# Performance work log

Measured on AMD Instinct MI355X. Metric: run time of the kernel, lower is better.

The kernel has to match this reference:

```python
import jax, jax.numpy as jnp
import numpy as np

N_NODES = 50000
N_EDGES = 800000
H = 128
LN_EPS = 1e-5


def setup_inputs() -> dict:
    key = jax.random.key(0)
    ks = jax.random.split(key, 8)
    x = jax.random.normal(ks[0], (N_NODES, H), dtype=jnp.float32)
    edge_index = jax.random.randint(ks[1], (2, N_EDGES), 0, N_NODES, dtype=jnp.int64)
    # edge_attention MLP params: Linear(2H -> H), ReLU, Linear(H -> 1), Sigmoid
    W1 = jax.random.normal(ks[2], (2 * H, H), dtype=jnp.float32) * 0.02
    b1 = jnp.zeros((H,), dtype=jnp.float32)
    W2 = jax.random.normal(ks[3], (H, 1), dtype=jnp.float32) * 0.02
    b2 = jnp.zeros((1,), dtype=jnp.float32)
    # LayerNorm affine params
    gamma = jnp.ones((H,), dtype=jnp.float32)
    beta = jnp.zeros((H,), dtype=jnp.float32)
    return {"x": x, "edge_index": edge_index, "W1": W1, "b1": b1,
            "W2": W2, "b2": b2, "gamma": gamma, "beta": beta}


def reference(x, edge_index, W1, b1, W2, b2, gamma, beta):
    src = edge_index[0]
    tgt = edge_index[1]
    # per-edge gated weight: sigmoid(MLP([x_src, x_tgt]))  -> [E]
    edge_feat = jnp.concatenate([x[src], x[tgt]], axis=1)        # [E, 2H]
    h = jax.nn.relu(edge_feat @ W1 + b1)                          # [E, H]
    w = jax.nn.sigmoid(h @ W2 + b2)[:, 0]                         # [E]
    # scatter-add weighted source features into targets (fused replacement
    # for the per-node Python loop in the original)
    agg = jax.ops.segment_sum(w[:, None] * x[src], tgt,
                              num_segments=x.shape[0])            # [N, H]
    attended = x + agg
    # LayerNorm over last dim
    mu = jnp.mean(attended, axis=-1, keepdims=True)
    var = jnp.mean(jnp.square(attended - mu), axis=-1, keepdims=True)
    out = (attended - mu) * jax.lax.rsqrt(var + LN_EPS) * gamma + beta
    return out
```

## Files before the change

### kernel.cpp

```cpp
#include <hip/hip_runtime.h>

static __device__ __forceinline__ unsigned short f2bf(float f) {
    union { float f; unsigned int u; } c; c.f = f;
    unsigned int u = c.u;
    return (unsigned short)((u + 0x7FFFu + ((u >> 16) & 1u)) >> 16);
}
static __device__ __forceinline__ float bflo(unsigned int uu) {
    union { unsigned int u; float f; } c; c.u = uu << 16; return c.f;
}
static __device__ __forceinline__ float bfhi(unsigned int uu) {
    union { unsigned int u; float f; } c; c.u = uu & 0xffff0000u; return c.f;
}
static __device__ __forceinline__ unsigned char f2fp8(float f) {
    int enc = __builtin_amdgcn_cvt_pk_fp8_f32(f, f, 0, false);
    return (unsigned char)(enc & 0xff);
}

typedef __bf16 bf16x8 __attribute__((ext_vector_type(8)));
typedef float  f32x4  __attribute__((ext_vector_type(4)));
typedef float  f32x2  __attribute__((ext_vector_type(2)));

#define SLOT      64
#define SPILLCAP  8192

static __device__ __forceinline__ float mlp16(uint4 ua, const float* __restrict__ vf,
                                              const float* __restrict__ w2r) {
    f32x2 d0 = __builtin_amdgcn_cvt_pk_f32_fp8(ua.x, false);
    f32x2 d1 = __builtin_amdgcn_cvt_pk_f32_fp8(ua.x, true);
    f32x2 d2 = __builtin_amdgcn_cvt_pk_f32_fp8(ua.y, false);
    f32x2 d3 = __builtin_amdgcn_cvt_pk_f32_fp8(ua.y, true);
    f32x2 d4 = __builtin_amdgcn_cvt_pk_f32_fp8(ua.z, false);
    f32x2 d5 = __builtin_amdgcn_cvt_pk_f32_fp8(ua.z, true);
    f32x2 d6 = __builtin_amdgcn_cvt_pk_f32_fp8(ua.w, false);
    f32x2 d7 = __builtin_amdgcn_cvt_pk_f32_fp8(ua.w, true);
    float p = 0.0f;
    p = fmaf(fmaxf(d0.x + vf[0],  0.f), w2r[0],  p);
    p = fmaf(fmaxf(d0.y + vf[1],  0.f), w2r[1],  p);
    p = fmaf(fmaxf(d1.x + vf[2],  0.f), w2r[2],  p);
    p = fmaf(fmaxf(d1.y + vf[3],  0.f), w2r[3],  p);
    p = fmaf(fmaxf(d2.x + vf[4],  0.f), w2r[4],  p);
    p = fmaf(fmaxf(d2.y + vf[5],  0.f), w2r[5],  p);
    p = fmaf(fmaxf(d3.x + vf[6],  0.f), w2r[6],  p);
    p = fmaf(fmaxf(d3.y + vf[7],  0.f), w2r[7],  p);
    p = fmaf(fmaxf(d4.x + vf[8],  0.f), w2r[8],  p);
    p = fmaf(fmaxf(d4.y + vf[9],  0.f), w2r[9],  p);
    p = fmaf(fmaxf(d5.x + vf[10], 0.f), w2r[10], p);
    p = fmaf(fmaxf(d5.y + vf[11], 0.f), w2r[11], p);
    p = fmaf(fmaxf(d6.x + vf[12], 0.f), w2r[12], p);
    p = fmaf(fmaxf(d6.y + vf[13], 0.f), w2r[13], p);
    p = fmaf(fmaxf(d7.x + vf[14], 0.f), w2r[14], p);
    p = fmaf(fmaxf(d7.y + vf[15], 0.f), w2r[15], p);
    return p;
}

__global__ void k_prep3(const float* __restrict__ W1, unsigned short* __restrict__ Bt,
                        const float* __restrict__ x, unsigned short* __restrict__ XB,
                        int* __restrict__ degnsp, int NH4, int N) {
    int idx = blockIdx.x * blockDim.x + threadIdx.x;
    int T = gridDim.x * blockDim.x;

    if (idx < 256 * 128) {
        int j = idx >> 7, k = idx & 127;
        int r = (j < 128) ? k : (128 + k);
        Bt[idx] = f2bf(W1[r * 128 + (j & 127)]);
    }

    for (int i = idx; i < NH4; i += T) {
        float4 f = ((const float4*)x)[i];
        ushort4 o;
        o.x = f2bf(f.x); o.y = f2bf(f.y); o.z = f2bf(f.z); o.w = f2bf(f.w);
        ((ushort4*)XB)[i] = o;
    }

    for (int i = idx; i <= N; i += T) degnsp[i] = 0;
}

template <typename IT>
__global__ __launch_bounds__(256) void k_gemmsc(const unsigned short* __restrict__ XB,
                                                const unsigned short* __restrict__ Bt,
                                                const float* __restrict__ b1,
                                                unsigned char* __restrict__ U,
                                                unsigned short* __restrict__ V,
                                                const int* __restrict__ ei,
                                                int* __restrict__ degnsp,
                                                IT* __restrict__ esrc2,
                                                int* __restrict__ spt,
                                                int* __restrict__ sps,
                                                int M, int E) {
    int wave = threadIdx.x >> 6, lane = threadIdx.x & 63;
    int row0 = blockIdx.x * 64 + wave * 16;
    int col0 = blockIdx.y * 64;
    int lr = lane & 15;
    int lk = (lane >> 4) << 3;

    f32x4 acc[4] = {};
    int arow = row0 + lr;
    bool in = (arow < M);
    const unsigned short* xr = XB + (size_t)arow * 128;

#pragma unroll
    for (int kk = 0; kk < 4; ++kk) {
        int k = kk * 32 + lk;
        bf16x8 a = {};
        if (in) a = *(const bf16x8*)(xr + k);
#pragma unroll
        for (int nf = 0; nf < 4; ++nf) {
            int col = col0 + nf * 16 + lr;
            bf16x8 b = *(const bf16x8*)(Bt + col * 128 + k);
            acc[nf] = __builtin_amdgcn_mfma_f32_16x16x32_bf16(a, b, acc[nf], 0, 0, 0);
        }
    }
    int rb = row0 + ((lane >> 4) << 2);
    if (col0 < 128) {
#pragma unroll
        for (int nf = 0; nf < 4; ++nf) {
            int feat = col0 + nf * 16 + lr;
#pragma unroll
            for (int r = 0; r < 4; ++r) {
                int node = rb + r;
                if (node < M) U[(size_t)node * 128 + feat] = f2fp8(acc[nf][r]);
            }
        }
    } else {
#pragma unroll
        for (int nf = 0; nf < 4; ++nf) {
            int feat = col0 + nf * 16 + lr - 128;
            float bias = b1[feat];
#pragma unroll
            for (int r = 0; r < 4; ++r) {
                int node = rb + r;
                if (node < M) V[(size_t)node * 128 + feat] = f2bf(acc[nf][r] + bias);
            }
        }
    }

    int gtid = ((blockIdx.y * gridDim.x + blockIdx.x) * blockDim.x) + threadIdx.x;
    int T = gridDim.x * gridDim.y * blockDim.x;
    int N = M;
    for (int e = gtid; e < E; e += T) {
        int s = ei[e];
        int t = ei[E + e];
        int r = atomicAdd(degnsp + t, 1);
        if (r < SLOT) {
            esrc2[((size_t)t << 6) + r] = (IT)s;
        } else {
            int sp = atomicAdd(degnsp + N, 1);
            if (sp < SPILLCAP) { spt[sp] = t; sps[sp] = s; }
        }
    }
}

template <typename IT>
__global__ __launch_bounds__(256) void k_fused_slot(const unsigned char* __restrict__ U,
                                                    const unsigned short* __restrict__ V,
                                                    const unsigned short* __restrict__ XB,
                                                    const int* __restrict__ degnsp,
                                                    const IT* __restrict__ esrc2,
                                                    const int* __restrict__ spt,
                                                    const int* __restrict__ sps,
                                                    const float* __restrict__ W2,
                                                    const float* __restrict__ b2,
                                                    const float* __restrict__ gamma,
                                                    const float* __restrict__ beta,
                                                    float* __restrict__ out, int N) {
    int row = blockIdx.x * 4 + (threadIdx.x >> 6);
    if (row >= N) return;
    int lane = threadIdx.x & 63;
    int el = lane & 7;
    int q  = lane >> 3;

    float w2r[16];
#pragma unroll
    for (int i = 0; i < 16; ++i) w2r[i] = W2[16 * q + i];
    float b2s = b2[0];

    const unsigned short* vp = V + (size_t)row * 128 + 16 * q;
    uint4 va = *(const uint4*)vp;
    uint4 vb = *(const uint4*)(vp + 8);
    float vf[16];
    vf[0]  = bflo(va.x); vf[1]  = bfhi(va.x);
    vf[2]  = bflo(va.y); vf[3]  = bfhi(va.y);
    vf[4]  = bflo(va.z); vf[5]  = bfhi(va.z);
    vf[6]  = bflo(va.w); vf[7]  = bfhi(va.w);
    vf[8]  = bflo(vb.x); vf[9]  = bfhi(vb.x);
    vf[10] = bflo(vb.y); vf[11] = bfhi(vb.y);
    vf[12] = bflo(vb.z); vf[13] = bfhi(vb.z);
    vf[14] = bflo(vb.w); vf[15] = bfhi(vb.w);

    int dg = degnsp[row];
    int st = row << 6;
    int en = st + (dg < SLOT ? dg : SLOT);

    unsigned int xvr = *(const unsigned int*)(XB + (size_t)row * 128 + 2 * lane);
    float a0 = bflo(xvr), a1 = bfhi(xvr);

    for (int g = st; g < en; g += 8) {
        int e = g + el;
        bool val = (e < en);
        int s = val ? (int)esrc2[e] : 0;

        uint4 ua = *(const uint4*)(U + (size_t)s * 128 + 16 * q);
        float p = mlp16(ua, vf, w2r);
        p += __shfl_xor(p, 8);
        p += __shfl_xor(p, 16);
        p += __shfl_xor(p, 32);
        float w = val ? 1.0f / (1.0f + __expf(-(p + b2s))) : 0.0f;

#pragma unroll
        for (int j = 0; j < 8; ++j) {
            float wj = __shfl(w, j);
            int   sj = __shfl(s, j);
            unsigned int xv = *(const unsigned int*)(XB + (size_t)sj * 128 + 2 * lane);
            a0 = fmaf(wj, bflo(xv), a0);
            a1 = fmaf(wj, bfhi(xv), a1);
        }
    }

    int ns = degnsp[N];
    if (ns > 0) {
        if (ns > SPILLCAP) ns = SPILLCAP;
        for (int i = 0; i < ns; ++i) {
            if (spt[i] == row) {
                int s = sps[i];
                uint4 ua = *(const uint4*)(U + (size_t)s * 128 + 16 * q);
                float p = mlp16(ua, vf, w2r);
                p += __shfl_xor(p, 8);
                p += __shfl_xor(p, 16);
                p += __shfl_xor(p, 32);
                float w = 1.0f / (1.0f + __expf(-(p + b2s)));
                unsigned int xv = *(const unsigned int*)(XB + (size_t)s * 128 + 2 * lane);
                a0 = fmaf(w, bflo(xv), a0);
                a1 = fmaf(w, bfhi(xv), a1);
            }
        }
    }

    float sm = a0 + a1;
#pragma unroll
    for (int off = 32; off; off >>= 1) sm += __shfl_xor(sm, off);
    float mu = sm * (1.0f / 128.0f);
    float d0v = a0 - mu, d1v = a1 - mu;
    float qq = d0v * d0v + d1v * d1v;
#pragma unroll
    for (int off = 32; off; off >>= 1) qq += __shfl_xor(qq, off);
    float rstd = rsqrtf(qq * (1.0f / 128.0f) + 1e-5f);
    float2 gg = *(const float2*)(gamma + 2 * lane);
    float2 bb = *(const float2*)(beta + 2 * lane);
    float2 o;
    o.x = d0v * rstd * gg.x + bb.x;
    o.y = d1v * rstd * gg.y + bb.y;
    *(float2*)(out + (size_t)row * 128 + 2 * lane) = o;
}

extern "C" void kernel_launch(void* const* d_in, const int* in_sizes, int n_in,
                              void* d_out, int out_size, void* d_ws, size_t ws_size,
                              hipStream_t stream) {
    const float* x     = (const float*)d_in[0];
    const int*   ei    = (const int*)d_in[1];
    const float* W1    = (const float*)d_in[2];
    const float* b1    = (const float*)d_in[3];
    const float* W2    = (const float*)d_in[4];
    const float* b2    = (const float*)d_in[5];
    const float* gamma = (const float*)d_in[6];
    const float* beta  = (const float*)d_in[7];
    float* out = (float*)d_out;

    const int N = in_sizes[0] / 128;
    const int E = in_sizes[1] / 2;

    char* w = (char*)d_ws;
    size_t off = 0;
    auto alloc = [&](size_t bytes) {
        char* p = w + off;
        off = (off + bytes + 255) & ~(size_t)255;
        return p;
    };
    unsigned short* Bt = (unsigned short*)alloc(256 * 128 * 2);
    unsigned char*  U  = (unsigned char*)alloc((size_t)N * 128);
    unsigned short* V  = (unsigned short*)alloc((size_t)N * 128 * 2);
    unsigned short* XB = (unsigned short*)alloc((size_t)N * 128 * 2);
    int* degnsp = (int*)alloc((size_t)(N + 1) * 4);
    int* spt    = (int*)alloc((size_t)SPILLCAP * 4);
    int* sps    = (int*)alloc((size_t)SPILLCAP * 4);

    bool small_idx = (N <= 65535);
    void* esrc2v;
    if (small_idx) esrc2v = alloc((size_t)N * SLOT * 2);
    else           esrc2v = alloc((size_t)N * SLOT * 4);

    k_prep3<<<2048, 256, 0, stream>>>(W1, Bt, x, XB, degnsp, N * 128 / 4, N);

    dim3 ggrid((N + 63) / 64, 4);
    if (small_idx) {
        unsigned short* esrc2 = (unsigned short*)esrc2v;
        k_gemmsc<unsigned short><<<ggrid, 256, 0, stream>>>(XB, Bt, b1, U, V, ei,
                                                            degnsp, esrc2, spt, sps,
                                                            N, E);
        k_fused_slot<unsigned short><<<(N + 3) / 4, 256, 0, stream>>>(
            U, V, XB, degnsp, esrc2, spt, sps, W2, b2, gamma, beta, out, N);
    } else {
        int* esrc2 = (int*)esrc2v;
        k_gemmsc<int><<<ggrid, 256, 0, stream>>>(XB, Bt, b1, U, V, ei,
                                                 degnsp, esrc2, spt, sps, N, E);
        k_fused_slot<int><<<(N + 3) / 4, 256, 0, stream>>>(
            U, V, XB, degnsp, esrc2, spt, sps, W2, b2, gamma, beta, out, N);
    }
}
```

Measured before the change: 152.4 us.

## Partition edge bucketing by target range per XCD with chunked work queues

The edge-to-slot scatter inside the GEMM kernel now reads the hardware XCC id. Each XCD owns one eighth of the target-node range and pulls 1024-edge chunks from its own atomic cursor, so the degree atomics and slot writes for a given node stay within one XCD's L2. The per-node counter atomics are relaxed to workgroup scope. In exchange every XCD scans the full target index array, and correctness now depends on the XCC id being in 0..7 and on these narrower-scope atomics being coherent across workgroups.

```diff
diff --git a/kernel.cpp b/kernel.cpp
--- a/kernel.cpp
+++ b/kernel.cpp
@@ -15,6 +15,11 @@
     int enc = __builtin_amdgcn_cvt_pk_fp8_f32(f, f, 0, false);
     return (unsigned char)(enc & 0xff);
 }
+static __device__ __forceinline__ int xcc_id() {
+    unsigned v;
+    asm volatile("s_getreg_b32 %0, hwreg(HW_REG_XCC_ID, 0, 32)" : "=s"(v));
+    return (int)(v & 7u);
+}
 
 typedef __bf16 bf16x8 __attribute__((ext_vector_type(8)));
 typedef float  f32x4  __attribute__((ext_vector_type(4)));
@@ -22,6 +27,8 @@
 
 #define SLOT      64
 #define SPILLCAP  8192
+#define NXCD      8
+#define CHUNK     1024
 
 static __device__ __forceinline__ float mlp16(uint4 ua, const float* __restrict__ vf,
                                               const float* __restrict__ w2r) {
@@ -55,7 +62,8 @@
 
 __global__ void k_prep3(const float* __restrict__ W1, unsigned short* __restrict__ Bt,
                         const float* __restrict__ x, unsigned short* __restrict__ XB,
-                        int* __restrict__ degnsp, int NH4, int N) {
+                        int* __restrict__ degnsp, int* __restrict__ cursor,
+                        int NH4, int N) {
     int idx = blockIdx.x * blockDim.x + threadIdx.x;
     int T = gridDim.x * blockDim.x;
 
@@ -64,6 +72,7 @@
         int r = (j < 128) ? k : (128 + k);
         Bt[idx] = f2bf(W1[r * 128 + (j & 127)]);
     }
+    if (idx < NXCD) cursor[idx] = 0;
 
     for (int i = idx; i < NH4; i += T) {
         float4 f = ((const float4*)x)[i];
@@ -83,6 +92,7 @@
                                                 unsigned short* __restrict__ V,
                                                 const int* __restrict__ ei,
                                                 int* __restrict__ degnsp,
+                                                int* __restrict__ cursor,
                                                 IT* __restrict__ esrc2,
                                                 int* __restrict__ spt,
                                                 int* __restrict__ sps,
@@ -134,18 +144,31 @@
         }
     }
 
-    int gtid = ((blockIdx.y * gridDim.x + blockIdx.x) * blockDim.x) + threadIdx.x;
-    int T = gridDim.x * gridDim.y * blockDim.x;
     int N = M;
-    for (int e = gtid; e < E; e += T) {
-        int s = ei[e];
-        int t = ei[E + e];
-        int r = atomicAdd(degnsp + t, 1);
-        if (r < SLOT) {
-            esrc2[((size_t)t << 6) + r] = (IT)s;
-        } else {
-            int sp = atomicAdd(degnsp + N, 1);
-            if (sp < SPILLCAP) { spt[sp] = t; sps[sp] = s; }
+    int cls = xcc_id();
+    int t0 = (int)(((long long)N * cls) >> 3);
+    int t1 = (int)(((long long)N * (cls + 1)) >> 3);
+    int nchunk = (E + CHUNK - 1) / CHUNK;
+
+    for (;;) {
+        int c;
+        if (lane == 0) c = atomicAdd(cursor + cls, 1);
+        c = __shfl(c, 0);
+        if (c >= nchunk) break;
+        int e0 = c * CHUNK;
+        int e1 = e0 + CHUNK; if (e1 > E) e1 = E;
+        for (int e = e0 + lane; e < e1; e += 64) {
+            int t = ei[E + e];
+            if (t < t0 || t >= t1) continue;
+            int s = ei[e];
+            int r = __hip_atomic_fetch_add(degnsp + t, 1, __ATOMIC_RELAXED,
+                                           __HIP_MEMORY_SCOPE_WORKGROUP);
+            if (r < SLOT) {
+                esrc2[((size_t)t << 6) + r] = (IT)s;
+            } else {
+                int sp = atomicAdd(degnsp + N, 1);
+                if (sp < SPILLCAP) { spt[sp] = t; sps[sp] = s; }
+            }
         }
     }
 }
@@ -280,6 +303,7 @@
     unsigned short* V  = (unsigned short*)alloc((size_t)N * 128 * 2);
     unsigned short* XB = (unsigned short*)alloc((size_t)N * 128 * 2);
     int* degnsp = (int*)alloc((size_t)(N + 1) * 4);
+    int* cursor = (int*)alloc(NXCD * 4);
     int* spt    = (int*)alloc((size_t)SPILLCAP * 4);
     int* sps    = (int*)alloc((size_t)SPILLCAP * 4);
 
@@ -288,20 +312,22 @@
     if (small_idx) esrc2v = alloc((size_t)N * SLOT * 2);
     else           esrc2v = alloc((size_t)N * SLOT * 4);
 
-    k_prep3<<<2048, 256, 0, stream>>>(W1, Bt, x, XB, degnsp, N * 128 / 4, N);
+    k_prep3<<<2048, 256, 0, stream>>>(W1, Bt, x, XB, degnsp, cursor,
+                                      N * 128 / 4, N);
 
     dim3 ggrid((N + 63) / 64, 4);
     if (small_idx) {
         unsigned short* esrc2 = (unsigned short*)esrc2v;
         k_gemmsc<unsigned short><<<ggrid, 256, 0, stream>>>(XB, Bt, b1, U, V, ei,
-                                                            degnsp, esrc2, spt, sps,
-                                                            N, E);
+                                                            degnsp, cursor, esrc2,
+                                                            spt, sps, N, E);
         k_fused_slot<unsigned short><<<(N + 3) / 4, 256, 0, stream>>>(
             U, V, XB, degnsp, esrc2, spt, sps, W2, b2, gamma, beta, out, N);
     } else {
         int* esrc2 = (int*)esrc2v;
         k_gemmsc<int><<<ggrid, 256, 0, stream>>>(XB, Bt, b1, U, V, ei,
-                                                 degnsp, esrc2, spt, sps, N, E);
+                                                 degnsp, cursor, esrc2,
+                                                 spt, sps, N, E);
         k_fused_slot<int><<<(N + 3) / 4, 256, 0, stream>>>(
             U, V, XB, degnsp, esrc2, spt, sps, W2, b2, gamma, beta, out, N);
     }
```

New measurement: 318.0 us (median of 2 runs). 109% more time.
